# Performance work log

Hardware: AMD Instinct MI355X
Metric: run time of the kernel (lower is better)

Reference implementation:

```python
import jax, jax.numpy as jnp
import numpy as np
from jax import lax

N_TAPS = 27  # 3x3x3 kernel

def _gather_one(xb, ti, hi, wi):
    # xb: (C,T,H,W); ti/hi/wi: (T,H,W) int32. Zero-fill outside bounds.
    C, T, H, W = xb.shape
    valid = (ti >= 0) & (ti < T) & (hi >= 0) & (hi < H) & (wi >= 0) & (wi < W)
    lin = (jnp.clip(ti, 0, T - 1) * H + jnp.clip(hi, 0, H - 1)) * W + jnp.clip(wi, 0, W - 1)
    v = jnp.take(xb.reshape(C, -1), lin.reshape(-1), axis=1).reshape(C, T, H, W)
    return v * valid.astype(xb.dtype)

_gather = jax.vmap(_gather_one)  # over batch

def _trilinear(x, t, h, w):
    # x: (B,C,T,H,W); t/h/w: (B,T,H,W) float sample coordinates.
    t0, h0, w0 = jnp.floor(t), jnp.floor(h), jnp.floor(w)
    lt, lh, lw = t - t0, h - h0, w - w0
    t0i, h0i, w0i = t0.astype(jnp.int32), h0.astype(jnp.int32), w0.astype(jnp.int32)
    acc = 0.0
    for ti, wt in ((t0i, 1.0 - lt), (t0i + 1, lt)):
        for hi, wh in ((h0i, 1.0 - lh), (h0i + 1, lh)):
            for wi, ww in ((w0i, 1.0 - lw), (w0i + 1, lw)):
                acc = acc + _gather(x, ti, hi, wi) * (wt * wh * ww)[:, None]
    return acc  # (B,C,T,H,W)

def _deform_conv3d(x, offset_w, offset_b, weight):
    # x: (B,Cin,T,H,W). Offset layout: (B, 3, 27, T, H, W), axis1=(dt,dh,dw),
    # tap index k = kt*9 + kh*3 + kw. stride=1, padding=1, dilation=1, no bias.
    off = lax.conv_general_dilated(
        x, offset_w, (1, 1, 1), [(1, 1)] * 3,
        dimension_numbers=("NCDHW", "OIDHW", "NCDHW"))
    off = off + offset_b[None, :, None, None, None]
    B, _, T, H, W = off.shape
    off = off.reshape(B, 3, N_TAPS, T, H, W)
    tg = jnp.arange(T, dtype=x.dtype)[:, None, None]
    hg = jnp.arange(H, dtype=x.dtype)[None, :, None]
    wg = jnp.arange(W, dtype=x.dtype)[None, None, :]
    out = jnp.zeros((B, weight.shape[0], T, H, W), x.dtype)
    for k in range(N_TAPS):
        kt, kh, kw = k // 9, (k // 3) % 3, k % 3
        t = tg + (kt - 1) + off[:, 0, k]
        h = hg + (kh - 1) + off[:, 1, k]
        w = wg + (kw - 1) + off[:, 2, k]
        s = _trilinear(x, t, h, w)  # (B,Cin,T,H,W)
        out = out + jnp.einsum('bcthw,oc->bothw', s, weight[:, :, kt, kh, kw])
    return out

def setup_inputs() -> dict:
    key = jax.random.key(0)
    ks = jax.random.split(key, 4)
    B, T, C, H, W = 1, 4, 64, 128, 128
    x = jax.random.normal(ks[0], (B, T, C, H, W), jnp.float32)
    # small init scale keeps predicted offsets in a realistic +-2px range
    offset_w = jax.random.normal(ks[1], (3 * N_TAPS, C, 3, 3, 3), jnp.float32) * 0.02
    offset_b = jnp.zeros((3 * N_TAPS,), jnp.float32)
    weight = jax.random.normal(ks[2], (C, C, 3, 3, 3), jnp.float32) * 0.02
    gamma = jax.random.normal(ks[3], (1,), jnp.float32) * 0.1
    return {"x": x, "offset_w": offset_w, "offset_b": offset_b,
            "weight": weight, "gamma": gamma}

def reference(x, offset_w, offset_b, weight, gamma):
    xp = jnp.transpose(x, (0, 2, 1, 3, 4))  # (B,C,T,H,W)
    xc = _deform_conv3d(xp, offset_w, offset_b, weight)
    return gamma[0] * jnp.transpose(xc, (0, 2, 1, 3, 4)) + x
```

## Files before the change

### kernel.cpp

```cpp
#include <hip/hip_runtime.h>
#include <cmath>

#define Cc 64
#define Hh 128
#define Ww 128
#define HW_ 16384
#define THW_ 65536
#define CHW_ 1048576
#define NT 27

typedef unsigned short ushort_t;
typedef _Float16 f16x2 __attribute__((ext_vector_type(2)));
typedef _Float16 f16x8 __attribute__((ext_vector_type(8)));
typedef __fp16 fp16x2_alt __attribute__((ext_vector_type(2)));
typedef float floatx4 __attribute__((ext_vector_type(4)));

union U32H2 { unsigned u; f16x2 h; };

static __device__ inline ushort_t f2h(float f) {
  union { _Float16 h; ushort_t u; } v;
  v.h = (_Float16)f;
  return v.u;
}

static __device__ inline unsigned pk2(float a) {
  union { fp16x2_alt h; unsigned u; } v;
  v.h = __builtin_amdgcn_cvt_pkrtz(a, a);
  return v.u;
}

#if defined(__has_builtin)
#if __has_builtin(__builtin_amdgcn_make_buffer_rsrc) && __has_builtin(__builtin_amdgcn_raw_buffer_load_b32)
#define USE_BUF 1
#endif
#endif
#ifndef USE_BUF
#define USE_BUF 0
#endif

struct XtBuf {
#if USE_BUF
  __amdgpu_buffer_rsrc_t r;
#else
  const unsigned* p;
#endif
};

static __device__ inline XtBuf mkbuf(const ushort_t* xt) {
  XtBuf b;
#if USE_BUF
  b.r = __builtin_amdgcn_make_buffer_rsrc((void*)xt, (short)0, 8388608, 0x00020000);
#else
  b.p = (const unsigned*)xt;
#endif
  return b;
}

static __device__ inline unsigned xload(const XtBuf& b, unsigned voff) {
#if USE_BUF
  return (unsigned)__builtin_amdgcn_raw_buffer_load_b32(b.r, (int)voff, 0, 0);
#else
  return b.p[voff >> 2];
#endif
}


__global__ __launch_bounds__(256) void prep(
    const float* __restrict__ offset_w,
    const float* __restrict__ weight,
    ushort_t* __restrict__ w2frag,
    ushort_t* __restrict__ wfrag)
{
  int e = blockIdx.x * 256 + threadIdx.x;
  if (e < 165888) {
    int j = e & 7, ln = (e >> 3) & 63, kh2 = (e >> 9) & 1, r = e >> 10;
    int ot = r % 6, k = r / 6;
    int oc = ot * 16 + (ln & 15);
    int c  = kh2 * 32 + (ln >> 4) * 8 + j;
    float v = (oc < 81) ? offset_w[(oc * 64 + c) * 27 + k] : 0.f;
    w2frag[e] = f2h(v);
  }
  if (e < 110592) {
    int j = e & 7, ln = (e >> 3) & 63, kh2 = (e >> 9) & 1, r = e >> 10;
    int ot = r & 3, k = r >> 2;
    int o = ot * 16 + (ln & 15);
    int c = kh2 * 32 + (ln >> 4) * 8 + j;
    wfrag[e] = f2h(weight[(o * 64 + c) * 27 + k]);
  }
}

__global__ __launch_bounds__(256) void transpose_x(
    const float* __restrict__ x, ushort_t* __restrict__ xt)
{
  __shared__ float tile[64][65];
  int b = blockIdx.x;
  int wblk = b & 1;
  int th = b >> 1;
  int h = th & 127;
  int t = th >> 7;
  int w0 = wblk * 64;
  int lane = threadIdx.x & 63;
  int quad = threadIdx.x >> 6;
  #pragma unroll
  for (int cc = 0; cc < 16; ++cc) {
    int c = cc * 4 + quad;
    tile[c][lane] = x[t * CHW_ + c * HW_ + h * Ww + w0 + lane];
  }
  __syncthreads();
  #pragma unroll
  for (int ww = 0; ww < 16; ++ww) {
    int w = ww * 4 + quad;
    xt[(size_t)(t * HW_ + h * Ww + w0 + w) * 64 + lane] = f2h(tile[lane][w]);
  }
}

__global__ __launch_bounds__(256, 4) void offconv(
    const ushort_t* __restrict__ xt,
    const ushort_t* __restrict__ w2frag,
    const float* __restrict__ ob,
    float* __restrict__ off)
{
  __shared__ __align__(16) char lds[24960];
  ushort_t* S = (ushort_t*)lds;
  float* Dbuf = (float*)lds;
  int lane = threadIdx.x & 63;
  int wavei = __builtin_amdgcn_readfirstlane(threadIdx.x >> 6);
  int quad = lane >> 4;
  int m16 = lane & 15;
  int hlf = lane >> 5;
  int lo4 = (lane & 31) * 4;
  int p0 = blockIdx.x * 64;
  int t = p0 >> 14;
  int h = (p0 >> 7) & 127;
  int w0 = p0 & 127;
  XtBuf xb = mkbuf(xt);

  floatx4 acc[6];
  #pragma unroll
  for (int i = 0; i < 6; ++i) acc[i] = (floatx4){0.f, 0.f, 0.f, 0.f};

  unsigned pd[8];

  auto issue = [&](int k) {
    int kt = k / 9, kh = (k / 3) % 3, kw = k % 3;
    int ts = t + kt - 1, hs = h + kh - 1;
    int tsc = min(max(ts, 0), 3);
    int hsc = min(max(hs, 0), 127);
    int sbase = tsc * HW_ + hsc * Ww;
    #pragma unroll
    for (int j = 0; j < 8; ++j) {
      int prow = wavei * 16 + j * 2 + hlf;
      int wc = w0 + prow + kw - 1;
      int wcc = min(max(wc, 0), 127);
      pd[j] = xload(xb, ((unsigned)(sbase + wcc) << 7) + lo4);
    }
  };

  issue(0);
  #pragma unroll 1
  for (int k = 0; k < NT; ++k) {
    int kt = k / 9, kh = (k / 3) % 3, kw = k % 3;
    int ts = t + kt - 1, hs = h + kh - 1;
    bool rowok = ((unsigned)ts < 4u) && ((unsigned)hs < 128u);
    #pragma unroll
    for (int j = 0; j < 8; ++j) {
      int prow = wavei * 16 + j * 2 + hlf;
      int wc = w0 + prow + kw - 1;
      bool ok = rowok && ((unsigned)wc < 128u);
      *(unsigned*)((char*)S + prow * 144 + lo4) = ok ? pd[j] : 0u;
    }
    issue(k + 1 < NT ? k + 1 : NT - 1);
    const ushort_t* srow = S + (wavei * 16 + m16) * 72 + quad * 8;
    f16x8 af0 = *(const f16x8*)srow;
    f16x8 af1 = *(const f16x8*)(srow + 32);
    #pragma unroll
    for (int ot = 0; ot < 6; ++ot) {
      const ushort_t* wb = w2frag + (size_t)((k * 6 + ot) * 2) * 512 + lane * 8;
      f16x8 b0 = *(const f16x8*)(wb);
      f16x8 b1 = *(const f16x8*)(wb + 512);
      acc[ot] = __builtin_amdgcn_mfma_f32_16x16x32_f16(af0, b0, acc[ot], 0, 0, 0);
      acc[ot] = __builtin_amdgcn_mfma_f32_16x16x32_f16(af1, b1, acc[ot], 0, 0, 0);
    }
  }
  __syncthreads();
  #pragma unroll
  for (int ot = 0; ot < 6; ++ot)
    #pragma unroll
    for (int r = 0; r < 4; ++r)
      Dbuf[(ot * 16 + m16) * 65 + wavei * 16 + quad * 4 + r] = acc[ot][r];
  __syncthreads();
  for (int i = threadIdx.x; i < 81 * 64; i += 256) {
    int oc = i >> 6, p = i & 63;
    off[(size_t)oc * THW_ + p0 + p] = Dbuf[oc * 65 + p] + ob[oc];
  }
}

__global__ __launch_bounds__(256, 4) void deform(
    const float* __restrict__ x,
    const ushort_t* __restrict__ xt,
    const float* __restrict__ off,
    const ushort_t* __restrict__ wfrag,
    const float* __restrict__ gamma,
    float* __restrict__ out)
{
  __shared__ __align__(16) char lds[16640];
  ushort_t* S = (ushort_t*)lds;
  unsigned* msite = (unsigned*)(lds + 9216);
  unsigned* mwt   = (unsigned*)(lds + 11264);
  float* Dbuf = (float*)lds;
  int lane = threadIdx.x & 63;
  int wavei = __builtin_amdgcn_readfirstlane(threadIdx.x >> 6);
  int quad = lane >> 4;
  int m16 = lane & 15;
  int hlf = lane >> 5;
  int lo4 = (lane & 31) * 4;
  int p0 = blockIdx.x * 64;
  int t = p0 >> 14;
  int h = (p0 >> 7) & 127;
  int w0 = p0 & 127;
  XtBuf xb = mkbuf(xt);

  floatx4 acc[4];
  #pragma unroll
  for (int i = 0; i < 4; ++i) acc[i] = (floatx4){0.f, 0.f, 0.f, 0.f};

  int pl = wavei * 16 + m16;
  int pm = p0 + pl;
  int aq = quad >> 1, bq = quad & 1;
  const float* offT = off + pm;

  float dt_c = offT[(size_t)(0 * NT + 0) * THW_];
  float dh_c = offT[(size_t)(1 * NT + 0) * THW_];
  float dw_c = offT[(size_t)(2 * NT + 0) * THW_];

  #pragma unroll 1
  for (int k = 0; k < NT; ++k) {
    int kn = (k + 1 < NT) ? k + 1 : NT - 1;
    float dt_n = offT[(size_t)(0 * NT + kn) * THW_];
    float dh_n = offT[(size_t)(1 * NT + kn) * THW_];
    float dw_n = offT[(size_t)(2 * NT + kn) * THW_];

    int kt = k / 9, kh = (k / 3) % 3, kw = k % 3;
    float tf = (float)(t + kt - 1) + dt_c;
    float hf = (float)(h + kh - 1) + dh_c;
    float wf = (float)(w0 + pl + kw - 1) + dw_c;
    float tF = floorf(tf), hF = floorf(hf), wF = floorf(wf);
    float lt = tf - tF, lh_ = hf - hF, lw_ = wf - wF;
    int t0 = (int)tF, h0 = (int)hF, wq_ = (int)wF;
    int ti = t0 + aq;
    float wt_ = (aq ? lt : 1.f - lt) * (((unsigned)ti < 4u) ? 1.f : 0.f);
    int tic = min(max(ti, 0), 3);
    int hi = h0 + bq;
    float wh_ = (bq ? lh_ : 1.f - lh_) * (((unsigned)hi < 128u) ? 1.f : 0.f);
    int hic = min(max(hi, 0), 127);
    int base2 = tic * HW_ + hic * Ww;
    float bw = wt_ * wh_;
    int wi0 = wq_;
    float ww0 = (1.f - lw_) * (((unsigned)wi0 < 128u) ? 1.f : 0.f);
    int wi0c = min(max(wi0, 0), 127);
    int wi1 = wq_ + 1;
    float ww1 = lw_ * (((unsigned)wi1 < 128u) ? 1.f : 0.f);
    int wi1c = min(max(wi1, 0), 127);
    uint2 sp_;
    sp_.x = (unsigned)(base2 + wi0c) << 7;
    sp_.y = (unsigned)(base2 + wi1c) << 7;
    *(uint2*)&msite[pl * 8 + quad * 2] = sp_;
    uint2 wp_;
    wp_.x = pk2(bw * ww0);
    wp_.y = pk2(bw * ww1);
    *(uint2*)&mwt[pl * 8 + quad * 2] = wp_;

    unsigned dreg[8][8];
    #pragma unroll
    for (int j = 0; j < 8; ++j) {
      int prow = wavei * 16 + j * 2 + hlf;
      const uint4* spp = (const uint4*)&msite[prow * 8];
      uint4 s03 = spp[0], s47 = spp[1];
      dreg[j][0] = xload(xb, s03.x + lo4);
      dreg[j][1] = xload(xb, s03.y + lo4);
      dreg[j][2] = xload(xb, s03.z + lo4);
      dreg[j][3] = xload(xb, s03.w + lo4);
      dreg[j][4] = xload(xb, s47.x + lo4);
      dreg[j][5] = xload(xb, s47.y + lo4);
      dreg[j][6] = xload(xb, s47.z + lo4);
      dreg[j][7] = xload(xb, s47.w + lo4);
    }
    #pragma unroll
    for (int j = 0; j < 8; ++j) {
      int prow = wavei * 16 + j * 2 + hlf;
      const uint4* wpp = (const uint4*)&mwt[prow * 8];
      uint4 w03 = wpp[0], w47 = wpp[1];
      U32H2 z; z.u = 0;
      f16x2 a2l = z.h, a2h = z.h;
      U32H2 du, wu;
      du.u = dreg[j][0]; wu.u = w03.x; a2l += wu.h * du.h;
      du.u = dreg[j][1]; wu.u = w03.y; a2h += wu.h * du.h;
      du.u = dreg[j][2]; wu.u = w03.z; a2l += wu.h * du.h;
      du.u = dreg[j][3]; wu.u = w03.w; a2h += wu.h * du.h;
      du.u = dreg[j][4]; wu.u = w47.x; a2l += wu.h * du.h;
      du.u = dreg[j][5]; wu.u = w47.y; a2h += wu.h * du.h;
      du.u = dreg[j][6]; wu.u = w47.z; a2l += wu.h * du.h;
      du.u = dreg[j][7]; wu.u = w47.w; a2h += wu.h * du.h;
      U32H2 res;
      res.h = a2l + a2h;
      *(unsigned*)((char*)S + prow * 144 + lo4) = res.u;
    }
    const ushort_t* srow = S + (wavei * 16 + m16) * 72 + quad * 8;
    f16x8 af0 = *(const f16x8*)srow;
    f16x8 af1 = *(const f16x8*)(srow + 32);
    #pragma unroll
    for (int ot = 0; ot < 4; ++ot) {
      const ushort_t* wb = wfrag + (size_t)((k * 4 + ot) * 2) * 512 + lane * 8;
      f16x8 b0 = *(const f16x8*)(wb);
      f16x8 b1 = *(const f16x8*)(wb + 512);
      acc[ot] = __builtin_amdgcn_mfma_f32_16x16x32_f16(af0, b0, acc[ot], 0, 0, 0);
      acc[ot] = __builtin_amdgcn_mfma_f32_16x16x32_f16(af1, b1, acc[ot], 0, 0, 0);
    }
    dt_c = dt_n; dh_c = dh_n; dw_c = dw_n;
  }
  __syncthreads();
  #pragma unroll
  for (int ot = 0; ot < 4; ++ot)
    #pragma unroll
    for (int r = 0; r < 4; ++r)
      Dbuf[(ot * 16 + m16) * 65 + wavei * 16 + quad * 4 + r] = acc[ot][r];
  __syncthreads();
  float g = gamma[0];
  for (int i = threadIdx.x; i < 64 * 64; i += 256) {
    int oc = i >> 6, p = i & 63;
    size_t oi = (size_t)t * CHW_ + (size_t)oc * HW_ + (size_t)h * Ww + w0 + p;
    out[oi] = fmaf(g, Dbuf[oc * 65 + p], x[oi]);
  }
}

extern "C" void kernel_launch(void* const* d_in, const int* in_sizes, int n_in,
                              void* d_out, int out_size, void* d_ws, size_t ws_size,
                              hipStream_t stream) {
  (void)in_sizes; (void)n_in; (void)out_size; (void)ws_size;
  const float* x        = (const float*)d_in[0];
  const float* offset_w = (const float*)d_in[1];
  const float* offset_b = (const float*)d_in[2];
  const float* weight   = (const float*)d_in[3];
  const float* gamma    = (const float*)d_in[4];
  float* out = (float*)d_out;
  float* wsf = (float*)d_ws;
  float*    off    = wsf;
  ushort_t* xt     = (ushort_t*)(wsf + 5308416);
  ushort_t* wfrag  = (ushort_t*)(wsf + 7405568);
  ushort_t* w2frag = (ushort_t*)(wsf + 7460864);

  hipLaunchKernelGGL(prep, dim3(648), dim3(256), 0, stream,
                     offset_w, weight, w2frag, wfrag);
  hipLaunchKernelGGL(transpose_x, dim3(1024), dim3(256), 0, stream, x, xt);
  hipLaunchKernelGGL(offconv, dim3(1024), dim3(256), 0, stream,
                     xt, w2frag, offset_b, off);
  hipLaunchKernelGGL(deform, dim3(1024), dim3(256), 0, stream,
                     x, xt, off, wfrag, gamma, out);
}
```

Baseline: 227.7 us.

## Split input channels across wave pairs and halve pixels per block

Both offconv and deform now process 32 pixels per block instead of 64. Each pair of waves splits the 64 input channels into two halves, each wave running one MFMA per output tile, and the partial sums are reduced through LDS. The grid doubles, LDS per block shrinks, launch bounds rise to 8 blocks per CU, and deform packs sample sites and weights into one per-wave uint4 table. The aim is more occupancy and fewer live registers to hide gather latency, at the cost of an extra LDS reduction step and duplicated offset and bilinear computation per pixel.

```diff
diff --git a/kernel.cpp b/kernel.cpp
--- a/kernel.cpp
+++ b/kernel.cpp
@@ -114,45 +114,46 @@
   }
 }
 
-__global__ __launch_bounds__(256, 4) void offconv(
+__global__ __launch_bounds__(256, 8) void offconv(
     const ushort_t* __restrict__ xt,
     const ushort_t* __restrict__ w2frag,
     const float* __restrict__ ob,
     float* __restrict__ off)
 {
-  __shared__ __align__(16) char lds[24960];
-  ushort_t* S = (ushort_t*)lds;
+  __shared__ __align__(16) char lds[13056];
   float* Dbuf = (float*)lds;
   int lane = threadIdx.x & 63;
   int wavei = __builtin_amdgcn_readfirstlane(threadIdx.x >> 6);
+  int pg = wavei >> 1;
+  int chh = wavei & 1;
   int quad = lane >> 4;
   int m16 = lane & 15;
-  int hlf = lane >> 5;
-  int lo4 = (lane & 31) * 4;
-  int p0 = blockIdx.x * 64;
+  int g = lane >> 4;
+  int c2 = lane & 15;
+  int p0 = blockIdx.x * 32;
   int t = p0 >> 14;
   int h = (p0 >> 7) & 127;
   int w0 = p0 & 127;
+  char* Sb = lds + wavei * 1280;
+  unsigned lanebyte = (unsigned)(chh * 64 + c2 * 4);
   XtBuf xb = mkbuf(xt);
 
   floatx4 acc[6];
   #pragma unroll
   for (int i = 0; i < 6; ++i) acc[i] = (floatx4){0.f, 0.f, 0.f, 0.f};
 
-  unsigned pd[8];
-
+  unsigned pd[4];
   auto issue = [&](int k) {
     int kt = k / 9, kh = (k / 3) % 3, kw = k % 3;
-    int ts = t + kt - 1, hs = h + kh - 1;
-    int tsc = min(max(ts, 0), 3);
-    int hsc = min(max(hs, 0), 127);
+    int tsc = min(max(t + kt - 1, 0), 3);
+    int hsc = min(max(h + kh - 1, 0), 127);
     int sbase = tsc * HW_ + hsc * Ww;
     #pragma unroll
-    for (int j = 0; j < 8; ++j) {
-      int prow = wavei * 16 + j * 2 + hlf;
-      int wc = w0 + prow + kw - 1;
+    for (int bq = 0; bq < 4; ++bq) {
+      int prow = bq * 4 + g;
+      int wc = w0 + pg * 16 + prow + kw - 1;
       int wcc = min(max(wc, 0), 127);
-      pd[j] = xload(xb, ((unsigned)(sbase + wcc) << 7) + lo4);
+      pd[bq] = xload(xb, ((unsigned)(sbase + wcc) << 7) + lanebyte);
     }
   };
 
@@ -160,42 +161,47 @@
   #pragma unroll 1
   for (int k = 0; k < NT; ++k) {
     int kt = k / 9, kh = (k / 3) % 3, kw = k % 3;
-    int ts = t + kt - 1, hs = h + kh - 1;
-    bool rowok = ((unsigned)ts < 4u) && ((unsigned)hs < 128u);
-    #pragma unroll
-    for (int j = 0; j < 8; ++j) {
-      int prow = wavei * 16 + j * 2 + hlf;
-      int wc = w0 + prow + kw - 1;
+    bool rowok = ((unsigned)(t + kt - 1) < 4u) && ((unsigned)(h + kh - 1) < 128u);
+    #pragma unroll
+    for (int bq = 0; bq < 4; ++bq) {
+      int prow = bq * 4 + g;
+      int wc = w0 + pg * 16 + prow + kw - 1;
       bool ok = rowok && ((unsigned)wc < 128u);
-      *(unsigned*)((char*)S + prow * 144 + lo4) = ok ? pd[j] : 0u;
+      *(unsigned*)(Sb + prow * 80 + c2 * 4) = ok ? pd[bq] : 0u;
     }
     issue(k + 1 < NT ? k + 1 : NT - 1);
-    const ushort_t* srow = S + (wavei * 16 + m16) * 72 + quad * 8;
-    f16x8 af0 = *(const f16x8*)srow;
-    f16x8 af1 = *(const f16x8*)(srow + 32);
+    f16x8 af = *(const f16x8*)(Sb + m16 * 80 + quad * 16);
     #pragma unroll
     for (int ot = 0; ot < 6; ++ot) {
-      const ushort_t* wb = w2frag + (size_t)((k * 6 + ot) * 2) * 512 + lane * 8;
-      f16x8 b0 = *(const f16x8*)(wb);
-      f16x8 b1 = *(const f16x8*)(wb + 512);
-      acc[ot] = __builtin_amdgcn_mfma_f32_16x16x32_f16(af0, b0, acc[ot], 0, 0, 0);
-      acc[ot] = __builtin_amdgcn_mfma_f32_16x16x32_f16(af1, b1, acc[ot], 0, 0, 0);
-    }
-  }
-  __syncthreads();
-  #pragma unroll
-  for (int ot = 0; ot < 6; ++ot)
-    #pragma unroll
-    for (int r = 0; r < 4; ++r)
-      Dbuf[(ot * 16 + m16) * 65 + wavei * 16 + quad * 4 + r] = acc[ot][r];
-  __syncthreads();
-  for (int i = threadIdx.x; i < 81 * 64; i += 256) {
-    int oc = i >> 6, p = i & 63;
-    off[(size_t)oc * THW_ + p0 + p] = Dbuf[oc * 65 + p] + ob[oc];
-  }
-}
-
-__global__ __launch_bounds__(256, 4) void deform(
+      const ushort_t* wb = w2frag + (size_t)((k * 6 + ot) * 2 + chh) * 512 + lane * 8;
+      f16x8 bf = *(const f16x8*)wb;
+      acc[ot] = __builtin_amdgcn_mfma_f32_16x16x32_f16(af, bf, acc[ot], 0, 0, 0);
+    }
+  }
+  __syncthreads();
+  if (chh == 0) {
+    #pragma unroll
+    for (int ot = 0; ot < 6; ++ot)
+      #pragma unroll
+      for (int r = 0; r < 4; ++r)
+        Dbuf[(ot * 16 + m16) * 34 + pg * 16 + quad * 4 + r] = acc[ot][r];
+  }
+  __syncthreads();
+  if (chh == 1) {
+    #pragma unroll
+    for (int ot = 0; ot < 6; ++ot)
+      #pragma unroll
+      for (int r = 0; r < 4; ++r)
+        Dbuf[(ot * 16 + m16) * 34 + pg * 16 + quad * 4 + r] += acc[ot][r];
+  }
+  __syncthreads();
+  for (int i = threadIdx.x; i < 81 * 32; i += 256) {
+    int oc = i >> 5, p = i & 31;
+    off[(size_t)oc * THW_ + p0 + p] = Dbuf[oc * 34 + p] + ob[oc];
+  }
+}
+
+__global__ __launch_bounds__(256, 8) void deform(
     const float* __restrict__ x,
     const ushort_t* __restrict__ xt,
     const float* __restrict__ off,
@@ -203,28 +209,30 @@
     const float* __restrict__ gamma,
     float* __restrict__ out)
 {
-  __shared__ __align__(16) char lds[16640];
-  ushort_t* S = (ushort_t*)lds;
-  unsigned* msite = (unsigned*)(lds + 9216);
-  unsigned* mwt   = (unsigned*)(lds + 11264);
+  __shared__ __align__(16) char lds[9216];
   float* Dbuf = (float*)lds;
   int lane = threadIdx.x & 63;
   int wavei = __builtin_amdgcn_readfirstlane(threadIdx.x >> 6);
+  int pg = wavei >> 1;
+  int chh = wavei & 1;
   int quad = lane >> 4;
   int m16 = lane & 15;
-  int hlf = lane >> 5;
-  int lo4 = (lane & 31) * 4;
-  int p0 = blockIdx.x * 64;
+  int g = lane >> 4;
+  int c2 = lane & 15;
+  int p0 = blockIdx.x * 32;
   int t = p0 >> 14;
   int h = (p0 >> 7) & 127;
   int w0 = p0 & 127;
+  char* Sb = lds + wavei * 2304;
+  char* Mt = Sb + 1280;
+  unsigned lanebyte = (unsigned)(chh * 64 + c2 * 4);
   XtBuf xb = mkbuf(xt);
 
   floatx4 acc[4];
   #pragma unroll
   for (int i = 0; i < 4; ++i) acc[i] = (floatx4){0.f, 0.f, 0.f, 0.f};
 
-  int pl = wavei * 16 + m16;
+  int pl = pg * 16 + m16;
   int pm = p0 + pl;
   int aq = quad >> 1, bq = quad & 1;
   const float* offT = off + pm;
@@ -261,75 +269,72 @@
     int wi1 = wq_ + 1;
     float ww1 = lw_ * (((unsigned)wi1 < 128u) ? 1.f : 0.f);
     int wi1c = min(max(wi1, 0), 127);
-    uint2 sp_;
-    sp_.x = (unsigned)(base2 + wi0c) << 7;
-    sp_.y = (unsigned)(base2 + wi1c) << 7;
-    *(uint2*)&msite[pl * 8 + quad * 2] = sp_;
-    uint2 wp_;
-    wp_.x = pk2(bw * ww0);
-    wp_.y = pk2(bw * ww1);
-    *(uint2*)&mwt[pl * 8 + quad * 2] = wp_;
-
-    unsigned dreg[8][8];
-    #pragma unroll
-    for (int j = 0; j < 8; ++j) {
-      int prow = wavei * 16 + j * 2 + hlf;
-      const uint4* spp = (const uint4*)&msite[prow * 8];
-      uint4 s03 = spp[0], s47 = spp[1];
-      dreg[j][0] = xload(xb, s03.x + lo4);
-      dreg[j][1] = xload(xb, s03.y + lo4);
-      dreg[j][2] = xload(xb, s03.z + lo4);
-      dreg[j][3] = xload(xb, s03.w + lo4);
-      dreg[j][4] = xload(xb, s47.x + lo4);
-      dreg[j][5] = xload(xb, s47.y + lo4);
-      dreg[j][6] = xload(xb, s47.z + lo4);
-      dreg[j][7] = xload(xb, s47.w + lo4);
-    }
-    #pragma unroll
-    for (int j = 0; j < 8; ++j) {
-      int prow = wavei * 16 + j * 2 + hlf;
-      const uint4* wpp = (const uint4*)&mwt[prow * 8];
-      uint4 w03 = wpp[0], w47 = wpp[1];
+    uint4 me;
+    me.x = (unsigned)(base2 + wi0c) << 7;
+    me.y = pk2(bw * ww0);
+    me.z = (unsigned)(base2 + wi1c) << 7;
+    me.w = pk2(bw * ww1);
+    *(uint4*)(Mt + m16 * 64 + quad * 16) = me;
+
+    #pragma unroll
+    for (int b2 = 0; b2 < 4; ++b2) {
+      int prow = b2 * 4 + g;
+      const uint4* mrow = (const uint4*)(Mt + prow * 64);
+      uint4 m01 = mrow[0], m23 = mrow[1], m45 = mrow[2], m67 = mrow[3];
+      unsigned d0 = xload(xb, m01.x + lanebyte);
+      unsigned d1 = xload(xb, m01.z + lanebyte);
+      unsigned d2 = xload(xb, m23.x + lanebyte);
+      unsigned d3 = xload(xb, m23.z + lanebyte);
+      unsigned d4 = xload(xb, m45.x + lanebyte);
+      unsigned d5 = xload(xb, m45.z + lanebyte);
+      unsigned d6 = xload(xb, m67.x + lanebyte);
+      unsigned d7 = xload(xb, m67.z + lanebyte);
       U32H2 z; z.u = 0;
       f16x2 a2l = z.h, a2h = z.h;
       U32H2 du, wu;
-      du.u = dreg[j][0]; wu.u = w03.x; a2l += wu.h * du.h;
-      du.u = dreg[j][1]; wu.u = w03.y; a2h += wu.h * du.h;
-      du.u = dreg[j][2]; wu.u = w03.z; a2l += wu.h * du.h;
-      du.u = dreg[j][3]; wu.u = w03.w; a2h += wu.h * du.h;
-      du.u = dreg[j][4]; wu.u = w47.x; a2l += wu.h * du.h;
-      du.u = dreg[j][5]; wu.u = w47.y; a2h += wu.h * du.h;
-      du.u = dreg[j][6]; wu.u = w47.z; a2l += wu.h * du.h;
-      du.u = dreg[j][7]; wu.u = w47.w; a2h += wu.h * du.h;
+      du.u = d0; wu.u = m01.y; a2l += wu.h * du.h;
+      du.u = d1; wu.u = m01.w; a2h += wu.h * du.h;
+      du.u = d2; wu.u = m23.y; a2l += wu.h * du.h;
+      du.u = d3; wu.u = m23.w; a2h += wu.h * du.h;
+      du.u = d4; wu.u = m45.y; a2l += wu.h * du.h;
+      du.u = d5; wu.u = m45.w; a2h += wu.h * du.h;
+      du.u = d6; wu.u = m67.y; a2l += wu.h * du.h;
+      du.u = d7; wu.u = m67.w; a2h += wu.h * du.h;
       U32H2 res;
       res.h = a2l + a2h;
-      *(unsigned*)((char*)S + prow * 144 + lo4) = res.u;
-    }
-    const ushort_t* srow = S + (wavei * 16 + m16) * 72 + quad * 8;
-    f16x8 af0 = *(const f16x8*)srow;
-    f16x8 af1 = *(const f16x8*)(srow + 32);
+      *(unsigned*)(Sb + prow * 80 + c2 * 4) = res.u;
+    }
+    f16x8 af = *(const f16x8*)(Sb + m16 * 80 + quad * 16);
     #pragma unroll
     for (int ot = 0; ot < 4; ++ot) {
-      const ushort_t* wb = wfrag + (size_t)((k * 4 + ot) * 2) * 512 + lane * 8;
-      f16x8 b0 = *(const f16x8*)(wb);
-      f16x8 b1 = *(const f16x8*)(wb + 512);
-      acc[ot] = __builtin_amdgcn_mfma_f32_16x16x32_f16(af0, b0, acc[ot], 0, 0, 0);
-      acc[ot] = __builtin_amdgcn_mfma_f32_16x16x32_f16(af1, b1, acc[ot], 0, 0, 0);
+      const ushort_t* wb = wfrag + (size_t)((k * 4 + ot) * 2 + chh) * 512 + lane * 8;
+      f16x8 bf = *(const f16x8*)wb;
+      acc[ot] = __builtin_amdgcn_mfma_f32_16x16x32_f16(af, bf, acc[ot], 0, 0, 0);
     }
     dt_c = dt_n; dh_c = dh_n; dw_c = dw_n;
   }
   __syncthreads();
-  #pragma unroll
-  for (int ot = 0; ot < 4; ++ot)
-    #pragma unroll
-    for (int r = 0; r < 4; ++r)
-      Dbuf[(ot * 16 + m16) * 65 + wavei * 16 + quad * 4 + r] = acc[ot][r];
-  __syncthreads();
-  float g = gamma[0];
-  for (int i = threadIdx.x; i < 64 * 64; i += 256) {
-    int oc = i >> 6, p = i & 63;
+  if (chh == 0) {
+    #pragma unroll
+    for (int ot = 0; ot < 4; ++ot)
+      #pragma unroll
+      for (int r = 0; r < 4; ++r)
+        Dbuf[(ot * 16 + m16) * 34 + pg * 16 + quad * 4 + r] = acc[ot][r];
+  }
+  __syncthreads();
+  if (chh == 1) {
+    #pragma unroll
+    for (int ot = 0; ot < 4; ++ot)
+      #pragma unroll
+      for (int r = 0; r < 4; ++r)
+        Dbuf[(ot * 16 + m16) * 34 + pg * 16 + quad * 4 + r] += acc[ot][r];
+  }
+  __syncthreads();
+  float gm = gamma[0];
+  for (int i = threadIdx.x; i < 64 * 32; i += 256) {
+    int oc = i >> 5, p = i & 31;
     size_t oi = (size_t)t * CHW_ + (size_t)oc * HW_ + (size_t)h * Ww + w0 + p;
-    out[oi] = fmaf(g, Dbuf[oc * 65 + p], x[oi]);
+    out[oi] = fmaf(gm, Dbuf[oc * 34 + p], x[oi]);
   }
 }
 
@@ -352,8 +357,8 @@
   hipLaunchKernelGGL(prep, dim3(648), dim3(256), 0, stream,
                      offset_w, weight, w2frag, wfrag);
   hipLaunchKernelGGL(transpose_x, dim3(1024), dim3(256), 0, stream, x, xt);
-  hipLaunchKernelGGL(offconv, dim3(1024), dim3(256), 0, stream,
+  hipLaunchKernelGGL(offconv, dim3(2048), dim3(256), 0, stream,
                      xt, w2frag, offset_b, off);
-  hipLaunchKernelGGL(deform, dim3(1024), dim3(256), 0, stream,
+  hipLaunchKernelGGL(deform, dim3(2048), dim3(256), 0, stream,
                      x, xt, off, wfrag, gamma, out);
 }
```

Measured after the change: 243.7 us. 7.0% more time.

## Load MFMA A-fragments directly from global with 128-bit loads, drop LDS staging

Applied to the files above, without the earlier changes.

Both the offset-conv and deform kernels now have each lane load its own MFMA A-operand fragment straight from the channel-last fp16 tensor using 16-byte buffer loads. This replaces the cooperative 32-bit loads that staged data through LDS. In deform, each lane computes all 8 trilinear corners for its own pixel and blends them in registers, instead of sharing site and weight tables through LDS. This removes LDS traffic and the LDS round-trip on every tap. The cost is more redundant address and weight arithmetic, higher register pressure, and dropping the explicit next-tap prefetch in offconv in favour of unroll-by-3. Out-of-bounds taps in offconv are zeroed by pointing the buffer load outside the resource range.

```diff
diff --git a/kernel.cpp b/kernel.cpp
--- a/kernel.cpp
+++ b/kernel.cpp
@@ -14,8 +14,10 @@
 typedef _Float16 f16x8 __attribute__((ext_vector_type(8)));
 typedef __fp16 fp16x2_alt __attribute__((ext_vector_type(2)));
 typedef float floatx4 __attribute__((ext_vector_type(4)));
+typedef unsigned uintx4 __attribute__((ext_vector_type(4)));
 
 union U32H2 { unsigned u; f16x2 h; };
+union B128 { uintx4 u; f16x8 h; };
 
 static __device__ inline ushort_t f2h(float f) {
   union { _Float16 h; ushort_t u; } v;
@@ -30,7 +32,7 @@
 }
 
 #if defined(__has_builtin)
-#if __has_builtin(__builtin_amdgcn_make_buffer_rsrc) && __has_builtin(__builtin_amdgcn_raw_buffer_load_b32)
+#if __has_builtin(__builtin_amdgcn_make_buffer_rsrc) && __has_builtin(__builtin_amdgcn_raw_buffer_load_b128)
 #define USE_BUF 1
 #endif
 #endif
@@ -42,7 +44,7 @@
 #if USE_BUF
   __amdgpu_buffer_rsrc_t r;
 #else
-  const unsigned* p;
+  const char* p;
 #endif
 };
 
@@ -51,16 +53,32 @@
 #if USE_BUF
   b.r = __builtin_amdgcn_make_buffer_rsrc((void*)xt, (short)0, 8388608, 0x00020000);
 #else
-  b.p = (const unsigned*)xt;
+  b.p = (const char*)xt;
 #endif
   return b;
 }
 
-static __device__ inline unsigned xload(const XtBuf& b, unsigned voff) {
+static __device__ inline uintx4 xload16m(const XtBuf& b, unsigned voff, bool ok) {
 #if USE_BUF
-  return (unsigned)__builtin_amdgcn_raw_buffer_load_b32(b.r, (int)voff, 0, 0);
+  unsigned vo = ok ? voff : 0x40000000u;
+  auto r = __builtin_amdgcn_raw_buffer_load_b128(b.r, (int)vo, 0, 0);
+  uintx4 v;
+  __builtin_memcpy(&v, &r, 16);
+  return v;
 #else
-  return b.p[voff >> 2];
+  uintx4 z = {0u, 0u, 0u, 0u};
+  return ok ? *(const uintx4*)(b.p + voff) : z;
+#endif
+}
+
+static __device__ inline uintx4 xload16(const XtBuf& b, unsigned voff) {
+#if USE_BUF
+  auto r = __builtin_amdgcn_raw_buffer_load_b128(b.r, (int)voff, 0, 0);
+  uintx4 v;
+  __builtin_memcpy(&v, &r, 16);
+  return v;
+#else
+  return *(const uintx4*)(b.p + voff);
 #endif
 }
 
@@ -120,15 +138,11 @@
     const float* __restrict__ ob,
     float* __restrict__ off)
 {
-  __shared__ __align__(16) char lds[24960];
-  ushort_t* S = (ushort_t*)lds;
-  float* Dbuf = (float*)lds;
+  __shared__ float Dbuf[96 * 65];
   int lane = threadIdx.x & 63;
   int wavei = __builtin_amdgcn_readfirstlane(threadIdx.x >> 6);
   int quad = lane >> 4;
   int m16 = lane & 15;
-  int hlf = lane >> 5;
-  int lo4 = (lane & 31) * 4;
   int p0 = blockIdx.x * 64;
   int t = p0 >> 14;
   int h = (p0 >> 7) & 127;
@@ -139,50 +153,29 @@
   #pragma unroll
   for (int i = 0; i < 6; ++i) acc[i] = (floatx4){0.f, 0.f, 0.f, 0.f};
 
-  unsigned pd[8];
-
-  auto issue = [&](int k) {
-    int kt = k / 9, kh = (k / 3) % 3, kw = k % 3;
-    int ts = t + kt - 1, hs = h + kh - 1;
-    int tsc = min(max(ts, 0), 3);
-    int hsc = min(max(hs, 0), 127);
-    int sbase = tsc * HW_ + hsc * Ww;
-    #pragma unroll
-    for (int j = 0; j < 8; ++j) {
-      int prow = wavei * 16 + j * 2 + hlf;
-      int wc = w0 + prow + kw - 1;
-      int wcc = min(max(wc, 0), 127);
-      pd[j] = xload(xb, ((unsigned)(sbase + wcc) << 7) + lo4);
-    }
-  };
-
-  issue(0);
-  #pragma unroll 1
+  #pragma unroll 3
   for (int k = 0; k < NT; ++k) {
     int kt = k / 9, kh = (k / 3) % 3, kw = k % 3;
     int ts = t + kt - 1, hs = h + kh - 1;
     bool rowok = ((unsigned)ts < 4u) && ((unsigned)hs < 128u);
-    #pragma unroll
-    for (int j = 0; j < 8; ++j) {
-      int prow = wavei * 16 + j * 2 + hlf;
-      int wc = w0 + prow + kw - 1;
-      bool ok = rowok && ((unsigned)wc < 128u);
-      *(unsigned*)((char*)S + prow * 144 + lo4) = ok ? pd[j] : 0u;
-    }
-    issue(k + 1 < NT ? k + 1 : NT - 1);
-    const ushort_t* srow = S + (wavei * 16 + m16) * 72 + quad * 8;
-    f16x8 af0 = *(const f16x8*)srow;
-    f16x8 af1 = *(const f16x8*)(srow + 32);
+    int tsc = min(max(ts, 0), 3);
+    int hsc = min(max(hs, 0), 127);
+    int wc = w0 + wavei * 16 + m16 + kw - 1;
+    bool ok = rowok && ((unsigned)wc < 128u);
+    int wcc = min(max(wc, 0), 127);
+    unsigned vo = ((unsigned)(tsc * HW_ + hsc * Ww + wcc) << 7) + (unsigned)(quad * 16);
+    B128 a0, a1;
+    a0.u = xload16m(xb, vo, ok);
+    a1.u = xload16m(xb, vo + 64, ok);
     #pragma unroll
     for (int ot = 0; ot < 6; ++ot) {
       const ushort_t* wb = w2frag + (size_t)((k * 6 + ot) * 2) * 512 + lane * 8;
       f16x8 b0 = *(const f16x8*)(wb);
       f16x8 b1 = *(const f16x8*)(wb + 512);
-      acc[ot] = __builtin_amdgcn_mfma_f32_16x16x32_f16(af0, b0, acc[ot], 0, 0, 0);
-      acc[ot] = __builtin_amdgcn_mfma_f32_16x16x32_f16(af1, b1, acc[ot], 0, 0, 0);
-    }
-  }
-  __syncthreads();
+      acc[ot] = __builtin_amdgcn_mfma_f32_16x16x32_f16(a0.h, b0, acc[ot], 0, 0, 0);
+      acc[ot] = __builtin_amdgcn_mfma_f32_16x16x32_f16(a1.h, b1, acc[ot], 0, 0, 0);
+    }
+  }
   #pragma unroll
   for (int ot = 0; ot < 6; ++ot)
     #pragma unroll
@@ -203,17 +196,11 @@
     const float* __restrict__ gamma,
     float* __restrict__ out)
 {
-  __shared__ __align__(16) char lds[16640];
-  ushort_t* S = (ushort_t*)lds;
-  unsigned* msite = (unsigned*)(lds + 9216);
-  unsigned* mwt   = (unsigned*)(lds + 11264);
-  float* Dbuf = (float*)lds;
+  __shared__ float Dbuf[64 * 65];
   int lane = threadIdx.x & 63;
   int wavei = __builtin_amdgcn_readfirstlane(threadIdx.x >> 6);
   int quad = lane >> 4;
   int m16 = lane & 15;
-  int hlf = lane >> 5;
-  int lo4 = (lane & 31) * 4;
   int p0 = blockIdx.x * 64;
   int t = p0 >> 14;
   int h = (p0 >> 7) & 127;
@@ -226,7 +213,6 @@
 
   int pl = wavei * 16 + m16;
   int pm = p0 + pl;
-  int aq = quad >> 1, bq = quad & 1;
   const float* offT = off + pm;
 
   float dt_c = offT[(size_t)(0 * NT + 0) * THW_];
@@ -247,78 +233,83 @@
     float tF = floorf(tf), hF = floorf(hf), wF = floorf(wf);
     float lt = tf - tF, lh_ = hf - hF, lw_ = wf - wF;
     int t0 = (int)tF, h0 = (int)hF, wq_ = (int)wF;
-    int ti = t0 + aq;
-    float wt_ = (aq ? lt : 1.f - lt) * (((unsigned)ti < 4u) ? 1.f : 0.f);
-    int tic = min(max(ti, 0), 3);
-    int hi = h0 + bq;
-    float wh_ = (bq ? lh_ : 1.f - lh_) * (((unsigned)hi < 128u) ? 1.f : 0.f);
-    int hic = min(max(hi, 0), 127);
-    int base2 = tic * HW_ + hic * Ww;
-    float bw = wt_ * wh_;
-    int wi0 = wq_;
-    float ww0 = (1.f - lw_) * (((unsigned)wi0 < 128u) ? 1.f : 0.f);
-    int wi0c = min(max(wi0, 0), 127);
-    int wi1 = wq_ + 1;
-    float ww1 = lw_ * (((unsigned)wi1 < 128u) ? 1.f : 0.f);
-    int wi1c = min(max(wi1, 0), 127);
-    uint2 sp_;
-    sp_.x = (unsigned)(base2 + wi0c) << 7;
-    sp_.y = (unsigned)(base2 + wi1c) << 7;
-    *(uint2*)&msite[pl * 8 + quad * 2] = sp_;
-    uint2 wp_;
-    wp_.x = pk2(bw * ww0);
-    wp_.y = pk2(bw * ww1);
-    *(uint2*)&mwt[pl * 8 + quad * 2] = wp_;
-
-    unsigned dreg[8][8];
-    #pragma unroll
-    for (int j = 0; j < 8; ++j) {
-      int prow = wavei * 16 + j * 2 + hlf;
-      const uint4* spp = (const uint4*)&msite[prow * 8];
-      uint4 s03 = spp[0], s47 = spp[1];
-      dreg[j][0] = xload(xb, s03.x + lo4);
-      dreg[j][1] = xload(xb, s03.y + lo4);
-      dreg[j][2] = xload(xb, s03.z + lo4);
-      dreg[j][3] = xload(xb, s03.w + lo4);
-      dreg[j][4] = xload(xb, s47.x + lo4);
-      dreg[j][5] = xload(xb, s47.y + lo4);
-      dreg[j][6] = xload(xb, s47.z + lo4);
-      dreg[j][7] = xload(xb, s47.w + lo4);
-    }
-    #pragma unroll
-    for (int j = 0; j < 8; ++j) {
-      int prow = wavei * 16 + j * 2 + hlf;
-      const uint4* wpp = (const uint4*)&mwt[prow * 8];
-      uint4 w03 = wpp[0], w47 = wpp[1];
+    float wtv[2], whv[2], wwv[2];
+    int tiv[2], hiv[2], wiv[2];
+    #pragma unroll
+    for (int a = 0; a < 2; ++a) {
+      int ti = t0 + a;
+      wtv[a] = (a ? lt : 1.f - lt) * (((unsigned)ti < 4u) ? 1.f : 0.f);
+      tiv[a] = min(max(ti, 0), 3);
+      int hi = h0 + a;
+      whv[a] = (a ? lh_ : 1.f - lh_) * (((unsigned)hi < 128u) ? 1.f : 0.f);
+      hiv[a] = min(max(hi, 0), 127);
+      int wi = wq_ + a;
+      wwv[a] = (a ? lw_ : 1.f - lw_) * (((unsigned)wi < 128u) ? 1.f : 0.f);
+      wiv[a] = min(max(wi, 0), 127);
+    }
+    unsigned vo[8], wk[8];
+    #pragma unroll
+    for (int a = 0; a < 2; ++a)
+      #pragma unroll
+      for (int b = 0; b < 2; ++b) {
+        int rowb = tiv[a] * HW_ + hiv[b] * Ww;
+        float rw = wtv[a] * whv[b];
+        #pragma unroll
+        for (int c = 0; c < 2; ++c) {
+          int idx = (a * 2 + b) * 2 + c;
+          vo[idx] = ((unsigned)(rowb + wiv[c]) << 7) + (unsigned)(quad * 16);
+          wk[idx] = pk2(rw * wwv[c]);
+        }
+      }
+    uintx4 d0[8];
+    #pragma unroll
+    for (int c = 0; c < 8; ++c) d0[c] = xload16(xb, vo[c]);
+    uintx4 d1[8];
+    #pragma unroll
+    for (int c = 0; c < 8; ++c) d1[c] = xload16(xb, vo[c] + 64);
+    B128 a0, a1;
+    {
       U32H2 z; z.u = 0;
-      f16x2 a2l = z.h, a2h = z.h;
-      U32H2 du, wu;
-      du.u = dreg[j][0]; wu.u = w03.x; a2l += wu.h * du.h;
-      du.u = dreg[j][1]; wu.u = w03.y; a2h += wu.h * du.h;
-      du.u = dreg[j][2]; wu.u = w03.z; a2l += wu.h * du.h;
-      du.u = dreg[j][3]; wu.u = w03.w; a2h += wu.h * du.h;
-      du.u = dreg[j][4]; wu.u = w47.x; a2l += wu.h * du.h;
-      du.u = dreg[j][5]; wu.u = w47.y; a2h += wu.h * du.h;
-      du.u = dreg[j][6]; wu.u = w47.z; a2l += wu.h * du.h;
-      du.u = dreg[j][7]; wu.u = w47.w; a2h += wu.h * du.h;
-      U32H2 res;
-      res.h = a2l + a2h;
-      *(unsigned*)((char*)S + prow * 144 + lo4) = res.u;
-    }
-    const ushort_t* srow = S + (wavei * 16 + m16) * 72 + quad * 8;
-    f16x8 af0 = *(const f16x8*)srow;
-    f16x8 af1 = *(const f16x8*)(srow + 32);
+      f16x2 s[4] = {z.h, z.h, z.h, z.h};
+      #pragma unroll
+      for (int c = 0; c < 8; ++c) {
+        U32H2 wu; wu.u = wk[c];
+        #pragma unroll
+        for (int q = 0; q < 4; ++q) {
+          U32H2 du; du.u = d0[c][q];
+          s[q] += wu.h * du.h;
+        }
+      }
+      U32H2 r0, r1, r2, r3;
+      r0.h = s[0]; r1.h = s[1]; r2.h = s[2]; r3.h = s[3];
+      a0.u = (uintx4){r0.u, r1.u, r2.u, r3.u};
+    }
+    {
+      U32H2 z; z.u = 0;
+      f16x2 s[4] = {z.h, z.h, z.h, z.h};
+      #pragma unroll
+      for (int c = 0; c < 8; ++c) {
+        U32H2 wu; wu.u = wk[c];
+        #pragma unroll
+        for (int q = 0; q < 4; ++q) {
+          U32H2 du; du.u = d1[c][q];
+          s[q] += wu.h * du.h;
+        }
+      }
+      U32H2 r0, r1, r2, r3;
+      r0.h = s[0]; r1.h = s[1]; r2.h = s[2]; r3.h = s[3];
+      a1.u = (uintx4){r0.u, r1.u, r2.u, r3.u};
+    }
     #pragma unroll
     for (int ot = 0; ot < 4; ++ot) {
       const ushort_t* wb = wfrag + (size_t)((k * 4 + ot) * 2) * 512 + lane * 8;
       f16x8 b0 = *(const f16x8*)(wb);
       f16x8 b1 = *(const f16x8*)(wb + 512);
-      acc[ot] = __builtin_amdgcn_mfma_f32_16x16x32_f16(af0, b0, acc[ot], 0, 0, 0);
-      acc[ot] = __builtin_amdgcn_mfma_f32_16x16x32_f16(af1, b1, acc[ot], 0, 0, 0);
+      acc[ot] = __builtin_amdgcn_mfma_f32_16x16x32_f16(a0.h, b0, acc[ot], 0, 0, 0);
+      acc[ot] = __builtin_amdgcn_mfma_f32_16x16x32_f16(a1.h, b1, acc[ot], 0, 0, 0);
     }
     dt_c = dt_n; dh_c = dh_n; dw_c = dw_n;
   }
-  __syncthreads();
   #pragma unroll
   for (int ot = 0; ot < 4; ++ot)
     #pragma unroll
```

New measurement: 367.0 us. +61.2%, slower.
